# Optimization experiments

Measured on AMD Instinct MI355X. Metric: run time of the kernel, lower is better.

The kernel has to match this reference:

```python
import jax, jax.numpy as jnp
import numpy as np

# dims: B=32 batch, F=40 max_frames, NB=36 num_boxes, R=512 region size, H=512 hidden
# feat_size D = R + 2H = 1536 ; relation attn input = 2D = 3072

def _soft_attention(feats, hidden, Wf, bf, Wh, bh, wa):
    # feats: (N, L, Din), hidden: (N, H) -> att feat (N, Din), alpha (N, L)
    e = jnp.tanh(feats @ Wf.T + bf + (hidden @ Wh.T + bh)[:, None, :]) @ wa  # (N, L)
    alpha = jax.nn.softmax(e, axis=1)
    att = jnp.einsum('nl,nld->nd', alpha, feats)
    return att, alpha


def setup_inputs() -> dict:
    key = jax.random.key(0)
    ks = jax.random.split(key, 16)
    B, F, NB, R, H = 32, 40, 36, 512, 512
    D = R + 2 * H  # 1536
    s = 0.02
    inp = {
        'i3d_feats': jax.random.normal(ks[0], (B, F, 2 * H), jnp.float32),
        'object_feats': jax.random.normal(ks[1], (B, F, NB, R), jnp.float32),
        'hidden_state': jax.random.normal(ks[2], (B, H), jnp.float32),
        # spatial SoftAttention(R, H, H)
        'Ws_f': jax.random.normal(ks[3], (H, R), jnp.float32) * s,
        'bs_f': jnp.zeros((H,), jnp.float32),
        'Ws_h': jax.random.normal(ks[4], (H, H), jnp.float32) * s,
        'bs_h': jnp.zeros((H,), jnp.float32),
        'was': jax.random.normal(ks[5], (H,), jnp.float32) * s,
        # relation SoftAttention(2D, H, H)
        'Wr_f': jax.random.normal(ks[6], (H, 2 * D), jnp.float32) * s,
        'br_f': jnp.zeros((H,), jnp.float32),
        'Wr_h': jax.random.normal(ks[7], (H, H), jnp.float32) * s,
        'br_h': jnp.zeros((H,), jnp.float32),
        'war': jax.random.normal(ks[8], (H,), jnp.float32) * s,
    }
    return inp


def reference(i3d_feats, object_feats, hidden_state,
              Ws_f, bs_f, Ws_h, bs_h, was,
              Wr_f, br_f, Wr_h, br_h, war):
    B, F, NB, R = object_feats.shape
    # ---- spatial attention over boxes (per frame) ----
    feats = object_feats.reshape(B * F, NB, R)
    hidden_rep = jnp.repeat(hidden_state, F, axis=0)  # == hidden.repeat(1,F).reshape(B*F,-1)
    obj_att, _ = _soft_attention(feats, hidden_rep, Ws_f, bs_f, Ws_h, bs_h, was)
    obj_att = obj_att.reshape(B, F, R)
    feat = jnp.concatenate([obj_att, i3d_feats], axis=-1)  # (B, F, D)
    D = feat.shape[-1]
    # ---- relation attention over all F*F frame pairs ----
    # pairwise[b, i*F + j] = concat(feat[b, j], feat[b, i])  (feat1 varies fast, feat2 slow)
    # Decompose Wr_f @ concat(fj, fi) = Wr1 @ fj + Wr2 @ fi to avoid O(F^2 * 2D) tensor.
    Wr1, Wr2 = Wr_f[:, :D], Wr_f[:, D:]
    p1 = feat @ Wr1.T  # (B, F, H), applied to fast index j
    p2 = feat @ Wr2.T  # (B, F, H), applied to slow index i
    hproj = hidden_state @ Wr_h.T + br_h  # (B, H)
    e = jnp.tanh(p2[:, :, None, :] + p1[:, None, :, :] + (hproj + br_f)[:, None, None, :]) @ war  # (B,F,F) [i,j]
    alpha = jax.nn.softmax(e.reshape(B, F * F), axis=1).reshape(B, F, F)
    # weighted sum of concat(feat[j], feat[i]) splits into two marginal sums
    rel1 = jnp.einsum('bij,bjd->bd', alpha, feat)
    rel2 = jnp.einsum('bij,bid->bd', alpha, feat)
    return jnp.concatenate([rel1, rel2], axis=-1)  # (B, 2D)
```

## Files before the change

### kernel.cpp

```cpp
#include <hip/hip_runtime.h>
#include <stdint.h>

#define B_SZ 32
#define F_SZ 40
#define NB_SZ 36
#define R_SZ 512
#define H_SZ 512
#define D_SZ 1536
#define M1 (B_SZ * F_SZ * NB_SZ)
#define NROW (B_SZ * F_SZ)
#define FNB (F_SZ * NB_SZ)

typedef __attribute__((ext_vector_type(8))) short short8;
typedef __attribute__((ext_vector_type(4))) float f32x4;

__device__ __forceinline__ unsigned short f2bf(float f) {
    unsigned int x = __float_as_uint(f);
    return (unsigned short)((x + 0x7fffu + ((x >> 16) & 1u)) >> 16);
}
__device__ __forceinline__ float bf2f(unsigned short u) {
    union { unsigned int i; float f; } v; v.i = ((unsigned int)u) << 16; return v.f;
}
__device__ __forceinline__ unsigned int cvtpk(float lo, float hi) {
    unsigned int r;
    asm("v_cvt_pk_bf16_f32 %0, %1, %2" : "=v"(r) : "v"(lo), "v"(hi));
    return r;
}
__device__ __forceinline__ float fast_rcp(float x) {
    float r; asm("v_rcp_f32 %0, %1" : "=v"(r) : "v"(x)); return r;
}
__device__ __forceinline__ float fast_tanh(float x) {
    float cx = fminf(fmaxf(x, -9.0f), 9.0f);
    float e = __expf(2.0f * cx);
    return (e - 1.0f) * fast_rcp(e + 1.0f);
}

__global__ __launch_bounds__(256) void k_cast(
    const float* __restrict__ Wsf, unsigned short* __restrict__ Wsb)
{
    int i = (blockIdx.x * 256 + threadIdx.x) * 8;
    float4 f0 = *(const float4*)(Wsf + i);
    float4 f1 = *(const float4*)(Wsf + i + 4);
    unsigned int u0 = cvtpk(f0.x, f0.y), u1 = cvtpk(f0.z, f0.w);
    unsigned int u2 = cvtpk(f1.x, f1.y), u3 = cvtpk(f1.z, f1.w);
    uint4 pk = {u0, u1, u2, u3};
    *(uint4*)(Wsb + i) = pk;
}

__global__ __launch_bounds__(256) void k_hproj(
    const float* __restrict__ hidden,
    const float* __restrict__ Wsh, const float* __restrict__ bsh,
    const float* __restrict__ bsf,
    const float* __restrict__ Wrh, const float* __restrict__ brh,
    const float* __restrict__ brf,
    float* __restrict__ hs, float* __restrict__ hr)
{
    __shared__ float hid[H_SZ];
    const int b = blockIdx.x >> 3, hc = blockIdx.x & 7;
    const int t = threadIdx.x;
    for (int i = t; i < H_SZ; i += 256) hid[i] = hidden[b * H_SZ + i];
    __syncthreads();
    const int h = hc * 64 + (t >> 2), kq = t & 3;
    const float* r1 = Wsh + (size_t)h * H_SZ + kq * 128;
    const float* r2 = Wrh + (size_t)h * H_SZ + kq * 128;
    const float* hh = hid + kq * 128;
    float a1 = 0.f, a2 = 0.f;
    for (int k = 0; k < 128; k += 4) {
        float4 v1 = *(const float4*)(r1 + k);
        float4 v2 = *(const float4*)(r2 + k);
        a1 += hh[k] * v1.x + hh[k+1] * v1.y + hh[k+2] * v1.z + hh[k+3] * v1.w;
        a2 += hh[k] * v2.x + hh[k+1] * v2.y + hh[k+2] * v2.z + hh[k+3] * v2.w;
    }
    a1 += __shfl_xor(a1, 1); a1 += __shfl_xor(a1, 2);
    a2 += __shfl_xor(a2, 1); a2 += __shfl_xor(a2, 2);
    if (kq == 0) {
        hs[b * H_SZ + h] = a1 + bsh[h] + bsf[h];
        hr[b * H_SZ + h] = a2 + brh[h] + brf[h];
    }
}

__global__ __launch_bounds__(256) void k_e1_mfma(
    const float* __restrict__ feats,
    const unsigned short* __restrict__ Wsb,
    const float* __restrict__ was,
    const float* __restrict__ hs,
    float* __restrict__ e1p)
{
    __shared__ __align__(16) unsigned char As[128 * 128];
    __shared__ __align__(16) unsigned char Bs[128 * 128];
    __shared__ float hsl[2 * 128];
    __shared__ float wasl[128];
    __shared__ float eps[2][128];

    const int bx = blockIdx.x;
    const int wid = (bx & 7) * 180 + (bx >> 3);
    const int mb = wid >> 2, by = wid & 3;
    const int m0 = mb * 128, hb = by * 128;
    const int t = threadIdx.x;
    const int b0 = m0 / FNB, b1 = (m0 + 127) / FNB;
    const int thr = (b0 + 1) * FNB - m0;

    if (t < 128) {
        hsl[t]       = hs[b0 * H_SZ + hb + t];
        hsl[128 + t] = hs[b1 * H_SZ + hb + t];
        wasl[t]      = was[hb + t];
    }

    const int lane = t & 63, w = t >> 6;
    const int wr = w >> 1, wc = w & 1;
    const int l15 = lane & 15, lk = lane >> 4;

    int aoff[4], boff[4];
#pragma unroll
    for (int i = 0; i < 4; i++) {
        int ra = wr * 64 + i * 16 + l15;
        aoff[i] = ra * 128 + (((lk) ^ (ra & 7)) << 4);
        int rb = wc * 64 + i * 16 + l15;
        boff[i] = rb * 128 + (((lk) ^ (rb & 7)) << 4);
    }
    int ar[4], br_[4];
#pragma unroll
    for (int i = 0; i < 4; i++) {
        ar[i]  = wr * 64 + i * 16 + l15;
        br_[i] = wc * 64 + i * 16 + l15;
    }

    float ep[4][4] = {{0.f}};
    f32x4 acc[4][4] = {};

    for (int k0 = 0; k0 < R_SZ; k0 += 64) {
        float4 alo[4], ahi[4];
        int4 bfr[4];
#pragma unroll
        for (int i = 0; i < 4; i++) {
            int cid = i * 256 + t;
            int r = cid >> 3, c = cid & 7;
            const float* src = feats + (size_t)(m0 + r) * R_SZ + k0 + c * 8;
            alo[i] = *(const float4*)src;
            ahi[i] = *(const float4*)(src + 4);
            bfr[i] = *(const int4*)(Wsb + (size_t)(hb + r) * R_SZ + k0 + c * 8);
        }
        __syncthreads();
#pragma unroll
        for (int i = 0; i < 4; i++) {
            int cid = i * 256 + t;
            int r = cid >> 3, c = cid & 7;
            unsigned int u0 = cvtpk(alo[i].x, alo[i].y), u1 = cvtpk(alo[i].z, alo[i].w);
            unsigned int u2 = cvtpk(ahi[i].x, ahi[i].y), u3 = cvtpk(ahi[i].z, ahi[i].w);
            uint4 pk = {u0, u1, u2, u3};
            int sw = (c ^ (r & 7)) << 4;
            *(uint4*)(As + r * 128 + sw) = pk;
            *(int4*)(Bs + r * 128 + sw) = bfr[i];
        }
        __syncthreads();
#pragma unroll
        for (int ks = 0; ks < 2; ks++) {
            short8 a[4], b[4];
#pragma unroll
            for (int i = 0; i < 4; i++) {
                int c = ks * 4 + lk;
                a[i] = *(const short8*)(As + ar[i] * 128 + ((c ^ (ar[i] & 7)) << 4));
                b[i] = *(const short8*)(Bs + br_[i] * 128 + ((c ^ (br_[i] & 7)) << 4));
            }
#pragma unroll
            for (int i = 0; i < 4; i++)
#pragma unroll
                for (int j = 0; j < 4; j++)
                    acc[i][j] = __builtin_amdgcn_mfma_f32_16x16x32_bf16(
                        a[i], b[j], acc[i][j], 0, 0, 0);
        }
    }

#pragma unroll
    for (int j = 0; j < 4; j++) {
        int hl = wc * 64 + j * 16 + l15;
        float wv = wasl[hl];
#pragma unroll
        for (int i = 0; i < 4; i++) {
#pragma unroll
            for (int q = 0; q < 4; q++) {
                int r = wr * 64 + i * 16 + lk * 4 + q;
                float hv = hsl[(r >= thr ? 128 : 0) + hl];
                ep[i][q] += fast_tanh(acc[i][j][q] + hv) * wv;
            }
        }
    }
#pragma unroll
    for (int i = 0; i < 4; i++)
#pragma unroll
        for (int q = 0; q < 4; q++) {
            float v = ep[i][q];
            v += __shfl_xor(v, 1);
            v += __shfl_xor(v, 2);
            v += __shfl_xor(v, 4);
            v += __shfl_xor(v, 8);
            if (l15 == 0) eps[wc][wr * 64 + i * 16 + lk * 4 + q] = v;
        }
    __syncthreads();
    if (t < 128) e1p[(size_t)by * M1 + m0 + t] = eps[0][t] + eps[1][t];
}

__global__ __launch_bounds__(256) void k_softatt(
    const float* __restrict__ feats,
    const float* __restrict__ i3d,
    const float* __restrict__ e1p,
    unsigned short* __restrict__ feat)
{
    __shared__ float alpha[NB_SZ];
    const int n = blockIdx.x, t = threadIdx.x;
    if (t < 64) {
        float v = -1e30f;
        if (t < NB_SZ) {
            int idx = n * NB_SZ + t;
            v = e1p[idx] + e1p[M1 + idx] + e1p[2 * M1 + idx] + e1p[3 * M1 + idx];
        }
        float m = v;
#pragma unroll
        for (int off = 32; off; off >>= 1) m = fmaxf(m, __shfl_xor(m, off));
        float ex = (t < NB_SZ) ? expf(v - m) : 0.f;
        float ssum = ex;
#pragma unroll
        for (int off = 32; off; off >>= 1) ssum += __shfl_xor(ssum, off);
        if (t < NB_SZ) alpha[t] = ex / ssum;
    }
    __syncthreads();

    float a0 = 0.f, a1 = 0.f;
    const float* base = feats + (size_t)n * NB_SZ * R_SZ;
    for (int ll = 0; ll < NB_SZ; ll++) {
        float al = alpha[ll];
        float2 pv = *(const float2*)(base + ll * R_SZ + 2 * t);
        a0 += al * pv.x;
        a1 += al * pv.y;
    }
    feat[(size_t)n * D_SZ + 2 * t]     = f2bf(a0);
    feat[(size_t)n * D_SZ + 2 * t + 1] = f2bf(a1);
    float4 iv = *(const float4*)(i3d + (size_t)n * 1024 + t * 4);
    unsigned short o[4] = {f2bf(iv.x), f2bf(iv.y), f2bf(iv.z), f2bf(iv.w)};
    *(uint2*)(feat + (size_t)n * D_SZ + 512 + t * 4) = *(const uint2*)o;
}

__global__ __launch_bounds__(256) void k_pgemm_mfma(
    const unsigned short* __restrict__ feat,
    const float* __restrict__ Wrf,
    float* __restrict__ p)
{
    __shared__ __align__(16) unsigned char As[64 * 256];
    __shared__ __align__(16) unsigned char Bs[64 * 256];

    const int bx = blockIdx.x;
    const int wid = (bx & 7) * 40 + (bx >> 3);
    const int mb = wid % 20, nb = wid / 20;
    const int m0 = mb * 64, j0 = nb * 64;
    const int t = threadIdx.x;

    const int lane = t & 63, w = t >> 6;
    const int wr = w >> 1, wc = w & 1;
    const int l15 = lane & 15, lk = lane >> 4;

    int ar[2], br_[2];
#pragma unroll
    for (int i = 0; i < 2; i++) {
        ar[i]  = wr * 32 + i * 16 + l15;
        br_[i] = wc * 32 + i * 16 + l15;
    }

    const size_t brow_base = (j0 < 512) ? (size_t)j0 * 3072 : ((size_t)(j0 - 512) * 3072 + 1536);

    f32x4 acc[2][2] = {};

    for (int k0 = 0; k0 < D_SZ; k0 += 128) {
        int4 afr[4];
        float4 blo[4], bhi[4];
#pragma unroll
        for (int i = 0; i < 4; i++) {
            int cid = i * 256 + t;
            int r = cid >> 4, c = cid & 15;
            afr[i] = *(const int4*)(feat + (size_t)(m0 + r) * D_SZ + k0 + c * 8);
            const float* bs = Wrf + brow_base + (size_t)r * 3072 + k0 + c * 8;
            blo[i] = *(const float4*)bs;
            bhi[i] = *(const float4*)(bs + 4);
        }
        __syncthreads();
#pragma unroll
        for (int i = 0; i < 4; i++) {
            int cid = i * 256 + t;
            int r = cid >> 4, c = cid & 15;
            int sw = (c ^ (r & 7)) << 4;
            *(int4*)(As + r * 256 + sw) = afr[i];
            unsigned int u0 = cvtpk(blo[i].x, blo[i].y), u1 = cvtpk(blo[i].z, blo[i].w);
            unsigned int u2 = cvtpk(bhi[i].x, bhi[i].y), u3 = cvtpk(bhi[i].z, bhi[i].w);
            uint4 pk = {u0, u1, u2, u3};
            *(uint4*)(Bs + r * 256 + sw) = pk;
        }
        __syncthreads();
#pragma unroll
        for (int ks = 0; ks < 4; ks++) {
            short8 a[2], b[2];
            int c = ks * 4 + lk;
#pragma unroll
            for (int i = 0; i < 2; i++) {
                a[i] = *(const short8*)(As + ar[i] * 256 + ((c ^ (ar[i] & 7)) << 4));
                b[i] = *(const short8*)(Bs + br_[i] * 256 + ((c ^ (br_[i] & 7)) << 4));
            }
#pragma unroll
            for (int i = 0; i < 2; i++)
#pragma unroll
                for (int j = 0; j < 2; j++)
                    acc[i][j] = __builtin_amdgcn_mfma_f32_16x16x32_bf16(
                        a[i], b[j], acc[i][j], 0, 0, 0);
        }
    }
#pragma unroll
    for (int i = 0; i < 2; i++)
#pragma unroll
        for (int j = 0; j < 2; j++)
#pragma unroll
            for (int q = 0; q < 4; q++) {
                int row = m0 + wr * 32 + i * 16 + lk * 4 + q;
                int col = j0 + wc * 32 + j * 16 + l15;
                p[(size_t)row * 1024 + col] = acc[i][j][q];
            }
}

__global__ __launch_bounds__(256) void k_e2(
    const float* __restrict__ p,
    const float* __restrict__ hr,
    const float* __restrict__ war,
    float* __restrict__ e2)
{
    const int blk = blockIdx.x;
    const int b = blk / F_SZ, i = blk % F_SZ;
    const int t = threadIdx.x;
    const int w = t >> 6, l = t & 63;
    const int ni = b * F_SZ + i;

    float base[8], warf[8];
    {
        float4 pa = *(const float4*)(p + (size_t)ni * 1024 + 512 + l * 8);
        float4 pb = *(const float4*)(p + (size_t)ni * 1024 + 512 + l * 8 + 4);
        float4 ha = *(const float4*)(hr + b * H_SZ + l * 8);
        float4 hb = *(const float4*)(hr + b * H_SZ + l * 8 + 4);
        base[0] = pa.x + ha.x; base[1] = pa.y + ha.y; base[2] = pa.z + ha.z; base[3] = pa.w + ha.w;
        base[4] = pb.x + hb.x; base[5] = pb.y + hb.y; base[6] = pb.z + hb.z; base[7] = pb.w + hb.w;
        float4 wa = *(const float4*)(war + l * 8);
        float4 wb = *(const float4*)(war + l * 8 + 4);
        warf[0] = wa.x; warf[1] = wa.y; warf[2] = wa.z; warf[3] = wa.w;
        warf[4] = wb.x; warf[5] = wb.y; warf[6] = wb.z; warf[7] = wb.w;
    }

    for (int j = w; j < F_SZ; j += 4) {
        const float* p1r = p + (size_t)(b * F_SZ + j) * 1024;
        float4 va = *(const float4*)(p1r + l * 8);
        float4 vb = *(const float4*)(p1r + l * 8 + 4);
        float pv[8] = {va.x, va.y, va.z, va.w, vb.x, vb.y, vb.z, vb.w};
        float s = 0.f;
#pragma unroll
        for (int u = 0; u < 8; u++) s += fast_tanh(pv[u] + base[u]) * warf[u];
#pragma unroll
        for (int off = 32; off; off >>= 1) s += __shfl_xor(s, off);
        if (l == 0) e2[(size_t)b * 1600 + i * F_SZ + j] = s;
    }
}

__global__ __launch_bounds__(256) void k_out(
    const float* __restrict__ e2,
    const unsigned short* __restrict__ feat,
    float* __restrict__ out)
{
    __shared__ float alpha[1600];
    __shared__ float red[4];
    __shared__ float rs[F_SZ], cs[F_SZ];
    const int b = blockIdx.x, t = threadIdx.x;
    const int w = t >> 6, l = t & 63;

    float lm = -1e30f;
    for (int idx = t; idx < 1600; idx += 256) {
        float v = e2[(size_t)b * 1600 + idx];
        alpha[idx] = v;
        lm = fmaxf(lm, v);
    }
#pragma unroll
    for (int off = 32; off; off >>= 1) lm = fmaxf(lm, __shfl_xor(lm, off));
    if (l == 0) red[w] = lm;
    __syncthreads();
    float M = fmaxf(fmaxf(red[0], red[1]), fmaxf(red[2], red[3]));
    __syncthreads();
    float ls = 0.f;
    for (int idx = t; idx < 1600; idx += 256) {
        float ex = expf(alpha[idx] - M);
        alpha[idx] = ex;
        ls += ex;
    }
#pragma unroll
    for (int off = 32; off; off >>= 1) ls += __shfl_xor(ls, off);
    if (l == 0) red[w] = ls;
    __syncthreads();
    float inv = 1.f / (red[0] + red[1] + red[2] + red[3]);

    if (t < F_SZ) {
        float s = 0.f;
        for (int j = 0; j < F_SZ; j++) s += alpha[t * F_SZ + j];
        rs[t] = s * inv;
    } else if (t >= 128 && t < 128 + F_SZ) {
        int j = t - 128;
        float s = 0.f;
        for (int i2 = 0; i2 < F_SZ; i2++) s += alpha[i2 * F_SZ + j];
        cs[j] = s * inv;
    }
    __syncthreads();

    float a1[6] = {0.f,0.f,0.f,0.f,0.f,0.f};
    float a2[6] = {0.f,0.f,0.f,0.f,0.f,0.f};
    for (int r = 0; r < F_SZ; r++) {
        float w1 = cs[r], w2 = rs[r];
        const unsigned short* fr = feat + (size_t)(b * F_SZ + r) * D_SZ;
#pragma unroll
        for (int u = 0; u < 6; u++) {
            float f = bf2f(fr[t + u * 256]);
            a1[u] += w1 * f;
            a2[u] += w2 * f;
        }
    }
#pragma unroll
    for (int u = 0; u < 6; u++) {
        out[(size_t)b * 3072 + t + u * 256]        = a1[u];
        out[(size_t)b * 3072 + 1536 + t + u * 256] = a2[u];
    }
}

extern "C" void kernel_launch(void* const* d_in, const int* in_sizes, int n_in,
                              void* d_out, int out_size, void* d_ws, size_t ws_size,
                              hipStream_t stream) {
    const float* i3d    = (const float*)d_in[0];
    const float* objf   = (const float*)d_in[1];
    const float* hidden = (const float*)d_in[2];
    const float* Wsf    = (const float*)d_in[3];
    const float* bsf    = (const float*)d_in[4];
    const float* Wsh    = (const float*)d_in[5];
    const float* bsh    = (const float*)d_in[6];
    const float* was    = (const float*)d_in[7];
    const float* Wrf    = (const float*)d_in[8];
    const float* brf    = (const float*)d_in[9];
    const float* Wrh    = (const float*)d_in[10];
    const float* brh    = (const float*)d_in[11];
    const float* war    = (const float*)d_in[12];
    float* out = (float*)d_out;

    char* ws = (char*)d_ws;
    float* hs  = (float*)(ws);
    float* hr  = (float*)(ws + 65536);
    float* p   = (float*)(ws + 131072);
    float* e1p = (float*)(ws + 131072);
    unsigned short* Wsb = (unsigned short*)(ws + 4849664);
    float* e2  = (float*)(ws + 5373952);
    unsigned short* feat = (unsigned short*)(ws + 5578752);

    k_cast<<<dim3(128), dim3(256), 0, stream>>>(Wsf, Wsb);
    k_hproj<<<dim3(256), dim3(256), 0, stream>>>(hidden, Wsh, bsh, bsf, Wrh, brh, brf, hs, hr);
    k_e1_mfma<<<dim3(1440), dim3(256), 0, stream>>>(objf, Wsb, was, hs, e1p);
    k_softatt<<<dim3(NROW), dim3(256), 0, stream>>>(objf, i3d, e1p, feat);
    k_pgemm_mfma<<<dim3(320), dim3(256), 0, stream>>>(feat, Wrf, p);
    k_e2<<<dim3(NROW), dim3(256), 0, stream>>>(p, hr, war, e2);
    k_out<<<dim3(B_SZ), dim3(256), 0, stream>>>(e2, feat, out);
}
```

Measured before the change: 327.5 us.

## Double-buffer GEMM tiles with direct global-to-LDS loads and merge prologue kernels

The two MFMA GEMM kernels (spatial e1 and relation projection) now double-buffer their LDS tiles. The bf16 operand is copied straight from global memory into LDS with global_load_lds, while the fp32 operand that needs conversion is prefetched into registers for the next k-step during compute. The relation GEMM is retiled to 64x32 with k-step 64, doubling its grid to 640 blocks for better CU occupancy. The weight-cast and hidden-projection kernels are merged into one launch to save a kernel launch. The cost is doubled LDS use per block and more register pressure, which can reduce occupancy.

```diff
diff --git a/kernel.cpp b/kernel.cpp
--- a/kernel.cpp
+++ b/kernel.cpp
@@ -35,29 +35,33 @@
     return (e - 1.0f) * fast_rcp(e + 1.0f);
 }
 
-__global__ __launch_bounds__(256) void k_cast(
-    const float* __restrict__ Wsf, unsigned short* __restrict__ Wsb)
-{
-    int i = (blockIdx.x * 256 + threadIdx.x) * 8;
-    float4 f0 = *(const float4*)(Wsf + i);
-    float4 f1 = *(const float4*)(Wsf + i + 4);
-    unsigned int u0 = cvtpk(f0.x, f0.y), u1 = cvtpk(f0.z, f0.w);
-    unsigned int u2 = cvtpk(f1.x, f1.y), u3 = cvtpk(f1.z, f1.w);
-    uint4 pk = {u0, u1, u2, u3};
-    *(uint4*)(Wsb + i) = pk;
-}
-
-__global__ __launch_bounds__(256) void k_hproj(
+__device__ __forceinline__ void gload_lds16(const void* gsrc, void* ldst) {
+    __builtin_amdgcn_global_load_lds(
+        (const __attribute__((address_space(1))) unsigned int*)gsrc,
+        (__attribute__((address_space(3))) unsigned int*)ldst, 16, 0, 0);
+}
+
+__global__ __launch_bounds__(256) void k_pre(
     const float* __restrict__ hidden,
     const float* __restrict__ Wsh, const float* __restrict__ bsh,
     const float* __restrict__ bsf,
     const float* __restrict__ Wrh, const float* __restrict__ brh,
     const float* __restrict__ brf,
-    float* __restrict__ hs, float* __restrict__ hr)
-{
+    float* __restrict__ hs, float* __restrict__ hr,
+    const float* __restrict__ Wsf, unsigned short* __restrict__ Wsb)
+{
+    const int t = threadIdx.x;
+    if (blockIdx.x >= 256) {
+        int i = ((blockIdx.x - 256) * 256 + t) * 8;
+        float4 f0 = *(const float4*)(Wsf + i);
+        float4 f1 = *(const float4*)(Wsf + i + 4);
+        uint4 pk = {cvtpk(f0.x, f0.y), cvtpk(f0.z, f0.w),
+                    cvtpk(f1.x, f1.y), cvtpk(f1.z, f1.w)};
+        *(uint4*)(Wsb + i) = pk;
+        return;
+    }
     __shared__ float hid[H_SZ];
     const int b = blockIdx.x >> 3, hc = blockIdx.x & 7;
-    const int t = threadIdx.x;
     for (int i = t; i < H_SZ; i += 256) hid[i] = hidden[b * H_SZ + i];
     __syncthreads();
     const int h = hc * 64 + (t >> 2), kq = t & 3;
@@ -86,8 +90,8 @@
     const float* __restrict__ hs,
     float* __restrict__ e1p)
 {
-    __shared__ __align__(16) unsigned char As[128 * 128];
-    __shared__ __align__(16) unsigned char Bs[128 * 128];
+    __shared__ __align__(16) unsigned char As[2][128 * 128];
+    __shared__ __align__(16) unsigned char Bs[2][128 * 128];
     __shared__ float hsl[2 * 128];
     __shared__ float wasl[128];
     __shared__ float eps[2][128];
@@ -110,65 +114,79 @@
     const int wr = w >> 1, wc = w & 1;
     const int l15 = lane & 15, lk = lane >> 4;
 
-    int aoff[4], boff[4];
-#pragma unroll
-    for (int i = 0; i < 4; i++) {
-        int ra = wr * 64 + i * 16 + l15;
-        aoff[i] = ra * 128 + (((lk) ^ (ra & 7)) << 4);
-        int rb = wc * 64 + i * 16 + l15;
-        boff[i] = rb * 128 + (((lk) ^ (rb & 7)) << 4);
-    }
-    int ar[4], br_[4];
+    int ar[4], brw[4];
 #pragma unroll
     for (int i = 0; i < 4; i++) {
         ar[i]  = wr * 64 + i * 16 + l15;
-        br_[i] = wc * 64 + i * 16 + l15;
-    }
-
+        brw[i] = wc * 64 + i * 16 + l15;
+    }
+
+    const int srow = t >> 3;
+    const int scol = t & 7;
+    const int wub  = (t & 192) * 16;
+
+    float4 alo[4], ahi[4];
+    f32x4 acc[4][4] = {};
     float ep[4][4] = {{0.f}};
-    f32x4 acc[4][4] = {};
-
-    for (int k0 = 0; k0 < R_SZ; k0 += 64) {
-        float4 alo[4], ahi[4];
-        int4 bfr[4];
-#pragma unroll
-        for (int i = 0; i < 4; i++) {
-            int cid = i * 256 + t;
-            int r = cid >> 3, c = cid & 7;
-            const float* src = feats + (size_t)(m0 + r) * R_SZ + k0 + c * 8;
-            alo[i] = *(const float4*)src;
-            ahi[i] = *(const float4*)(src + 4);
-            bfr[i] = *(const int4*)(Wsb + (size_t)(hb + r) * R_SZ + k0 + c * 8);
-        }
+
+#define E1_LOAD_A(K0) do { \
+    _Pragma("unroll") \
+    for (int it = 0; it < 4; it++) { \
+        int r = it * 32 + srow; \
+        const float* src = feats + (size_t)(m0 + r) * R_SZ + (K0) + scol * 8; \
+        alo[it] = *(const float4*)src; \
+        ahi[it] = *(const float4*)(src + 4); \
+    } } while (0)
+
+#define E1_STAGE_B(BUF, K0) do { \
+    _Pragma("unroll") \
+    for (int it = 0; it < 4; it++) { \
+        int r = it * 32 + srow; \
+        int gc = scol ^ (r & 7); \
+        gload_lds16(Wsb + (size_t)(hb + r) * R_SZ + (K0) + gc * 8, \
+                    &Bs[BUF][it * 4096 + wub]); \
+    } } while (0)
+
+#define E1_WRITE_A(BUF) do { \
+    _Pragma("unroll") \
+    for (int it = 0; it < 4; it++) { \
+        int r = it * 32 + srow; \
+        uint4 pk = {cvtpk(alo[it].x, alo[it].y), cvtpk(alo[it].z, alo[it].w), \
+                    cvtpk(ahi[it].x, ahi[it].y), cvtpk(ahi[it].z, ahi[it].w)}; \
+        *(uint4*)(&As[BUF][r * 128 + ((scol ^ (r & 7)) << 4)]) = pk; \
+    } } while (0)
+
+#define E1_COMPUTE(BUF) do { \
+    _Pragma("unroll") \
+    for (int ks = 0; ks < 2; ks++) { \
+        short8 a[4], bv[4]; \
+        int c = ks * 4 + lk; \
+        _Pragma("unroll") \
+        for (int i = 0; i < 4; i++) { \
+            a[i]  = *(const short8*)(&As[BUF][ar[i]  * 128 + ((c ^ (ar[i]  & 7)) << 4)]); \
+            bv[i] = *(const short8*)(&Bs[BUF][brw[i] * 128 + ((c ^ (brw[i] & 7)) << 4)]); \
+        } \
+        _Pragma("unroll") \
+        for (int i = 0; i < 4; i++) \
+        _Pragma("unroll") \
+        for (int j = 0; j < 4; j++) \
+            acc[i][j] = __builtin_amdgcn_mfma_f32_16x16x32_bf16(a[i], bv[j], acc[i][j], 0, 0, 0); \
+    } } while (0)
+
+    E1_LOAD_A(0);
+    E1_STAGE_B(0, 0);
+    E1_WRITE_A(0);
+    __syncthreads();
+
+    for (int ki = 0; ki < 8; ki++) {
+        int cur = ki & 1, nxt = cur ^ 1;
+        if (ki < 7) {
+            E1_LOAD_A((ki + 1) * 64);
+            E1_STAGE_B(nxt, (ki + 1) * 64);
+        }
+        E1_COMPUTE(cur);
+        if (ki < 7) E1_WRITE_A(nxt);
         __syncthreads();
-#pragma unroll
-        for (int i = 0; i < 4; i++) {
-            int cid = i * 256 + t;
-            int r = cid >> 3, c = cid & 7;
-            unsigned int u0 = cvtpk(alo[i].x, alo[i].y), u1 = cvtpk(alo[i].z, alo[i].w);
-            unsigned int u2 = cvtpk(ahi[i].x, ahi[i].y), u3 = cvtpk(ahi[i].z, ahi[i].w);
-            uint4 pk = {u0, u1, u2, u3};
-            int sw = (c ^ (r & 7)) << 4;
-            *(uint4*)(As + r * 128 + sw) = pk;
-            *(int4*)(Bs + r * 128 + sw) = bfr[i];
-        }
-        __syncthreads();
-#pragma unroll
-        for (int ks = 0; ks < 2; ks++) {
-            short8 a[4], b[4];
-#pragma unroll
-            for (int i = 0; i < 4; i++) {
-                int c = ks * 4 + lk;
-                a[i] = *(const short8*)(As + ar[i] * 128 + ((c ^ (ar[i] & 7)) << 4));
-                b[i] = *(const short8*)(Bs + br_[i] * 128 + ((c ^ (br_[i] & 7)) << 4));
-            }
-#pragma unroll
-            for (int i = 0; i < 4; i++)
-#pragma unroll
-                for (int j = 0; j < 4; j++)
-                    acc[i][j] = __builtin_amdgcn_mfma_f32_16x16x32_bf16(
-                        a[i], b[j], acc[i][j], 0, 0, 0);
-        }
     }
 
 #pragma unroll
@@ -198,6 +216,10 @@
         }
     __syncthreads();
     if (t < 128) e1p[(size_t)by * M1 + m0 + t] = eps[0][t] + eps[1][t];
+#undef E1_LOAD_A
+#undef E1_STAGE_B
+#undef E1_WRITE_A
+#undef E1_COMPUTE
 }
 
 __global__ __launch_bounds__(256) void k_softatt(
@@ -245,82 +267,93 @@
     const float* __restrict__ Wrf,
     float* __restrict__ p)
 {
-    __shared__ __align__(16) unsigned char As[64 * 256];
-    __shared__ __align__(16) unsigned char Bs[64 * 256];
+    __shared__ __align__(16) unsigned char As[2][64 * 128];
+    __shared__ __align__(16) unsigned char Bs[2][32 * 128];
 
     const int bx = blockIdx.x;
-    const int wid = (bx & 7) * 40 + (bx >> 3);
+    const int wid = (bx & 7) * 80 + (bx >> 3);
     const int mb = wid % 20, nb = wid / 20;
-    const int m0 = mb * 64, j0 = nb * 64;
+    const int m0 = mb * 64, j0 = nb * 32;
     const int t = threadIdx.x;
 
     const int lane = t & 63, w = t >> 6;
     const int wr = w >> 1, wc = w & 1;
     const int l15 = lane & 15, lk = lane >> 4;
 
-    int ar[2], br_[2];
-#pragma unroll
-    for (int i = 0; i < 2; i++) {
-        ar[i]  = wr * 32 + i * 16 + l15;
-        br_[i] = wc * 32 + i * 16 + l15;
-    }
-
-    const size_t brow_base = (j0 < 512) ? (size_t)j0 * 3072 : ((size_t)(j0 - 512) * 3072 + 1536);
-
-    f32x4 acc[2][2] = {};
-
-    for (int k0 = 0; k0 < D_SZ; k0 += 128) {
-        int4 afr[4];
-        float4 blo[4], bhi[4];
-#pragma unroll
-        for (int i = 0; i < 4; i++) {
-            int cid = i * 256 + t;
-            int r = cid >> 4, c = cid & 15;
-            afr[i] = *(const int4*)(feat + (size_t)(m0 + r) * D_SZ + k0 + c * 8);
-            const float* bs = Wrf + brow_base + (size_t)r * 3072 + k0 + c * 8;
-            blo[i] = *(const float4*)bs;
-            bhi[i] = *(const float4*)(bs + 4);
-        }
+    const int srow = t >> 3;
+    const int scol = t & 7;
+    const int wub  = (t & 192) * 16;
+
+    const size_t brow_base = (j0 < 512) ? (size_t)j0 * 3072
+                                        : ((size_t)(j0 - 512) * 3072 + 1536);
+
+    int ar[2];
+    ar[0] = wr * 32 + l15; ar[1] = ar[0] + 16;
+    const int brow = wc * 16 + l15;
+
+    float4 blo, bhi;
+    f32x4 acc[2] = {};
+
+#define PG_STAGE_A(BUF, K0) do { \
+    _Pragma("unroll") \
+    for (int it = 0; it < 2; it++) { \
+        int r = it * 32 + srow; \
+        int gc = scol ^ (r & 7); \
+        gload_lds16(feat + (size_t)(m0 + r) * D_SZ + (K0) + gc * 8, \
+                    &As[BUF][it * 4096 + wub]); \
+    } } while (0)
+
+#define PG_LOAD_B(K0) do { \
+    const float* src = Wrf + brow_base + (size_t)srow * 3072 + (K0) + scol * 8; \
+    blo = *(const float4*)src; \
+    bhi = *(const float4*)(src + 4); \
+    } while (0)
+
+#define PG_WRITE_B(BUF) do { \
+    uint4 pk = {cvtpk(blo.x, blo.y), cvtpk(blo.z, blo.w), \
+                cvtpk(bhi.x, bhi.y), cvtpk(bhi.z, bhi.w)}; \
+    *(uint4*)(&Bs[BUF][srow * 128 + ((scol ^ (srow & 7)) << 4)]) = pk; \
+    } while (0)
+
+#define PG_COMPUTE(BUF) do { \
+    _Pragma("unroll") \
+    for (int ks = 0; ks < 2; ks++) { \
+        int c = ks * 4 + lk; \
+        short8 a0 = *(const short8*)(&As[BUF][ar[0] * 128 + ((c ^ (ar[0] & 7)) << 4)]); \
+        short8 a1 = *(const short8*)(&As[BUF][ar[1] * 128 + ((c ^ (ar[1] & 7)) << 4)]); \
+        short8 bv = *(const short8*)(&Bs[BUF][brow  * 128 + ((c ^ (brow  & 7)) << 4)]); \
+        acc[0] = __builtin_amdgcn_mfma_f32_16x16x32_bf16(a0, bv, acc[0], 0, 0, 0); \
+        acc[1] = __builtin_amdgcn_mfma_f32_16x16x32_bf16(a1, bv, acc[1], 0, 0, 0); \
+    } } while (0)
+
+    PG_LOAD_B(0);
+    PG_STAGE_A(0, 0);
+    PG_WRITE_B(0);
+    __syncthreads();
+
+    for (int ki = 0; ki < 24; ki++) {
+        int cur = ki & 1, nxt = cur ^ 1;
+        if (ki < 23) {
+            PG_LOAD_B((ki + 1) * 64);
+            PG_STAGE_A(nxt, (ki + 1) * 64);
+        }
+        PG_COMPUTE(cur);
+        if (ki < 23) PG_WRITE_B(nxt);
         __syncthreads();
-#pragma unroll
-        for (int i = 0; i < 4; i++) {
-            int cid = i * 256 + t;
-            int r = cid >> 4, c = cid & 15;
-            int sw = (c ^ (r & 7)) << 4;
-            *(int4*)(As + r * 256 + sw) = afr[i];
-            unsigned int u0 = cvtpk(blo[i].x, blo[i].y), u1 = cvtpk(blo[i].z, blo[i].w);
-            unsigned int u2 = cvtpk(bhi[i].x, bhi[i].y), u3 = cvtpk(bhi[i].z, bhi[i].w);
-            uint4 pk = {u0, u1, u2, u3};
-            *(uint4*)(Bs + r * 256 + sw) = pk;
-        }
-        __syncthreads();
-#pragma unroll
-        for (int ks = 0; ks < 4; ks++) {
-            short8 a[2], b[2];
-            int c = ks * 4 + lk;
-#pragma unroll
-            for (int i = 0; i < 2; i++) {
-                a[i] = *(const short8*)(As + ar[i] * 256 + ((c ^ (ar[i] & 7)) << 4));
-                b[i] = *(const short8*)(Bs + br_[i] * 256 + ((c ^ (br_[i] & 7)) << 4));
-            }
-#pragma unroll
-            for (int i = 0; i < 2; i++)
-#pragma unroll
-                for (int j = 0; j < 2; j++)
-                    acc[i][j] = __builtin_amdgcn_mfma_f32_16x16x32_bf16(
-                        a[i], b[j], acc[i][j], 0, 0, 0);
-        }
-    }
+    }
+
 #pragma unroll
     for (int i = 0; i < 2; i++)
 #pragma unroll
-        for (int j = 0; j < 2; j++)
-#pragma unroll
-            for (int q = 0; q < 4; q++) {
-                int row = m0 + wr * 32 + i * 16 + lk * 4 + q;
-                int col = j0 + wc * 32 + j * 16 + l15;
-                p[(size_t)row * 1024 + col] = acc[i][j][q];
-            }
+        for (int q = 0; q < 4; q++) {
+            int row = m0 + wr * 32 + i * 16 + lk * 4 + q;
+            int col = j0 + wc * 16 + l15;
+            p[(size_t)row * 1024 + col] = acc[i][q];
+        }
+#undef PG_STAGE_A
+#undef PG_LOAD_B
+#undef PG_WRITE_B
+#undef PG_COMPUTE
 }
 
 __global__ __launch_bounds__(256) void k_e2(
@@ -456,11 +489,10 @@
     float* e2  = (float*)(ws + 5373952);
     unsigned short* feat = (unsigned short*)(ws + 5578752);
 
-    k_cast<<<dim3(128), dim3(256), 0, stream>>>(Wsf, Wsb);
-    k_hproj<<<dim3(256), dim3(256), 0, stream>>>(hidden, Wsh, bsh, bsf, Wrh, brh, brf, hs, hr);
+    k_pre<<<dim3(384), dim3(256), 0, stream>>>(hidden, Wsh, bsh, bsf, Wrh, brh, brf, hs, hr, Wsf, Wsb);
     k_e1_mfma<<<dim3(1440), dim3(256), 0, stream>>>(objf, Wsb, was, hs, e1p);
     k_softatt<<<dim3(NROW), dim3(256), 0, stream>>>(objf, i3d, e1p, feat);
-    k_pgemm_mfma<<<dim3(320), dim3(256), 0, stream>>>(feat, Wrf, p);
+    k_pgemm_mfma<<<dim3(640), dim3(256), 0, stream>>>(feat, Wrf, p);
     k_e2<<<dim3(NROW), dim3(256), 0, stream>>>(p, hr, war, e2);
     k_out<<<dim3(B_SZ), dim3(256), 0, stream>>>(e2, feat, out);
 }
```

New measurement: 284.7 us. -13.1%, faster.
